# Kernel tuning notes

Measured on AMD Instinct MI355X. Metric: run time of the kernel, lower is better.

## Reference

```python
import jax, jax.numpy as jnp
import numpy as np

B = 8192
FL = 96      # feature_len
K = 3        # dynamic filter kernel size
NOUT = 2
EPS = 1e-5
P = (K - 1) // 2

def _lrelu(x):
    return jnp.where(x >= 0, x, 0.1 * x)

def _conv1d(x, w, b):
    # x: [b,1,L], w: [1,1,3], b: [1]; padding=1, stride=1
    y = jax.lax.conv_general_dilated(x, w, (1,), [(1, 1)], dimension_numbers=('NCH', 'OIH', 'NCH'))
    return y + b[None, :, None]

def _bn(y, g, be, m, v):
    # eval-mode BatchNorm1d with running stats
    return (y - m) / jnp.sqrt(v + EPS) * g + be


def setup_inputs() -> dict:
    key = jax.random.key(0)
    ks = jax.random.split(key, 40)
    d = {'x': jax.random.normal(ks[0], (B, 576), jnp.float32)}
    # trans_layer: 6 conv1d (1->1, k=3)
    for i in range(6):
        d[f'cw{i+1}'] = jax.random.normal(ks[1 + i], (1, 1, 3), jnp.float32) * 0.4
        d[f'cb{i+1}'] = jax.random.normal(ks[7 + i], (1,), jnp.float32) * 0.1
    # fusion_layer.de_dimen: Linear(FL -> K*K)
    d['de_W'] = jax.random.normal(ks[13], (K * K, FL), jnp.float32) * 0.1
    d['de_b'] = jnp.zeros((K * K,), jnp.float32)
    # reshape_layer: Linear(2*FL -> 3*FL) + BN
    d['rs_W'] = jax.random.normal(ks[14], (3 * FL, 2 * FL), jnp.float32) * 0.07
    d['rs_b'] = jnp.zeros((3 * FL,), jnp.float32)
    d['rs_g'] = 1.0 + 0.1 * jax.random.normal(ks[15], (3 * FL,), jnp.float32)
    d['rs_be'] = 0.1 * jax.random.normal(ks[16], (3 * FL,), jnp.float32)
    d['rs_m'] = 0.05 * jax.random.normal(ks[17], (3 * FL,), jnp.float32)
    d['rs_v'] = jax.random.uniform(ks[18], (3 * FL,), jnp.float32, 0.5, 1.5)
    # classifier_shallow: Linear(6*FL -> 3*FL) + BN + ReLU + Linear(3*FL -> NOUT)
    d['cl_W1'] = jax.random.normal(ks[19], (3 * FL, 6 * FL), jnp.float32) * 0.05
    d['cl_b1'] = jnp.zeros((3 * FL,), jnp.float32)
    d['cl_g'] = 1.0 + 0.1 * jax.random.normal(ks[20], (3 * FL,), jnp.float32)
    d['cl_be'] = 0.1 * jax.random.normal(ks[21], (3 * FL,), jnp.float32)
    d['cl_m'] = 0.05 * jax.random.normal(ks[22], (3 * FL,), jnp.float32)
    d['cl_v'] = jax.random.uniform(ks[23], (3 * FL,), jnp.float32, 0.5, 1.5)
    d['cl_W2'] = jax.random.normal(ks[24], (NOUT, 3 * FL), jnp.float32) * 0.05
    d['cl_b2'] = jnp.zeros((NOUT,), jnp.float32)
    return d


def reference(x, cw1, cb1, cw2, cb2, cw3, cb3, cw4, cb4, cw5, cb5, cw6, cb6,
              de_W, de_b, rs_W, rs_b, rs_g, rs_be, rs_m, rs_v,
              cl_W1, cl_b1, cl_g, cl_be, cl_m, cl_v, cl_W2, cl_b2):
    def trans(c):  # c: [b,1,3*FL] -> three [b,1,FL]
        s1, s2, s3 = c[..., :FL], c[..., FL:2 * FL], c[..., 2 * FL:]
        x1 = _lrelu(_conv1d(s1, cw1, cb1))
        x2 = _lrelu(_conv1d(s2, cw2, cb2))
        x3 = _lrelu(_conv1d(s3, cw3, cb3))
        return (_lrelu(_conv1d(x1, cw4, cb4)),
                _lrelu(_conv1d(x2, cw5, cb5)),
                _lrelu(_conv1d(x3, cw6, cb6)))

    def fusion(arm, x86, bert):  # each [b,1,FL]
        b = arm.shape[0]
        # c==1 so matmul(s_1^T, s_2) is a per-sample outer product: [b,FL,FL]
        m = _lrelu(jnp.einsum('bl,bm->blm', arm[:, 0], x86[:, 0]))
        # per-sample 3x3 dynamic filter from bert embedding
        s3 = _lrelu(bert[:, 0] @ de_W.T + de_b).reshape(b, 1, K, K)
        fe = jax.lax.conv_general_dilated(
            m.reshape(1, b, FL, FL), s3, (1, 1), [(P, P), (P, P)],
            feature_group_count=b, dimension_numbers=('NCHW', 'OIHW', 'NCHW'))
        fe = _lrelu(fe).reshape(b, FL, FL)
        # AvgPool1d(FL) == mean over last dim (and over rows for the permuted map)
        return jnp.concatenate([fe.mean(axis=2), fe.mean(axis=1)], axis=1)  # [b,2*FL]

    def resh(e):
        return _lrelu(_bn(e @ rs_W.T + rs_b, rs_g, rs_be, rs_m, rs_v))

    xu = x[:, None, :]  # unsqueeze(dim=1)
    c1, c2 = xu[..., :3 * FL], xu[..., 3 * FL:]
    e1 = resh(fusion(*trans(c1))) + c1[:, 0]
    e2 = resh(fusion(*trans(c2))) + c2[:, 0]
    ce = jnp.concatenate([e1, e2], axis=1)  # [b,6*FL]
    # Dropout is identity in eval mode
    h = jax.nn.relu(_bn(ce @ cl_W1.T + cl_b1, cl_g, cl_be, cl_m, cl_v))
    return h @ cl_W2.T + cl_b2  # [b,NOUT]
```

## Files before the change

kernel.cpp:

```cpp
#include <hip/hip_runtime.h>
#include <hip/hip_bf16.h>
#include <math.h>

#define FLn 96
#define SEG 288
#define EPRE_DIM 192
#define EPS_BN 1e-5f

typedef __attribute__((ext_vector_type(8))) short short8;
typedef __attribute__((ext_vector_type(4))) float floatx4;

__device__ __forceinline__ float lrelu(float v) { return fmaxf(v, 0.1f * v); }
__device__ __forceinline__ short f2bf(float f) {
  __hip_bfloat16 h = __float2bfloat16(f);
  return *reinterpret_cast<short*>(&h);
}

__global__ __launch_bounds__(256) void k0_swz(
    const float* __restrict__ rsW, const float* __restrict__ clW1,
    short* __restrict__ wB2s, short* __restrict__ wB3s) {
  int idx = blockIdx.x * 256 + threadIdx.x;
  int stride = gridDim.x * 256;
  for (int d = idx; d < 18 * 6 * 512; d += stride) {
    int j = d & 7, lane = (d >> 3) & 63, t = d >> 9;
    int kf = t % 6, nf = t / 6;
    int n = nf * 16 + (lane & 15);
    int k = kf * 32 + (lane >> 4) * 8 + j;
    wB2s[d] = f2bf(rsW[n * 192 + k]);
  }
  for (int d = idx; d < 18 * 18 * 512; d += stride) {
    int j = d & 7, lane = (d >> 3) & 63, t = d >> 9;
    int kf = t % 18, nt = t / 18;
    int n = nt * 16 + (lane & 15);
    int k = kf * 32 + (lane >> 4) * 8 + j;
    wB3s[d] = f2bf(clW1[n * 576 + k]);
  }
}

#define O_CIN 0
#define O_ST1 288
#define O_APP 576
#define O_ANP 674
#define O_XPP 772
#define O_XNP 870
#define O_BERT 968
#define O_WKER 1064
#define O_ABF 1088
#define O_BBF 1472
#define O_RP 0
#define SLICE 2048

__global__ __launch_bounds__(256) void k1_persample(
    const float* __restrict__ x,
    const float* __restrict__ cw1, const float* __restrict__ cb1,
    const float* __restrict__ cw2, const float* __restrict__ cb2,
    const float* __restrict__ cw3, const float* __restrict__ cb3,
    const float* __restrict__ cw4, const float* __restrict__ cb4,
    const float* __restrict__ cw5, const float* __restrict__ cb5,
    const float* __restrict__ cw6, const float* __restrict__ cb6,
    const float* __restrict__ deW, const float* __restrict__ deb,
    short* __restrict__ epre_s) {
  __shared__ float sl[4 * SLICE];
  const int tid = threadIdx.x;
  const int wave = tid >> 6;
  const int lane = tid & 63;
  const int quad = lane >> 4;
  const int l16 = lane & 15;
  const int unit = blockIdx.x * 4 + wave;
  float* S = sl + wave * SLICE;
  short* Ssh = (short*)S;
  const float* xrow = x + (size_t)(unit >> 1) * 576 + (unit & 1) * 288;

  const float a0w0 = cw1[0], a0w1 = cw1[1], a0w2 = cw1[2], a0b = cb1[0];
  const float a1w0 = cw2[0], a1w1 = cw2[1], a1w2 = cw2[2], a1b = cb2[0];
  const float a2w0 = cw3[0], a2w1 = cw3[1], a2w2 = cw3[2], a2b = cb3[0];
  const float b0w0 = cw4[0], b0w1 = cw4[1], b0w2 = cw4[2], b0b = cb4[0];
  const float b1w0 = cw5[0], b1w1 = cw5[1], b1w2 = cw5[2], b1b = cb5[0];
  const float b2w0 = cw6[0], b2w1 = cw6[1], b2w2 = cw6[2], b2b = cb6[0];

  for (int t4 = lane; t4 < 72; t4 += 64)
    *(float4*)&S[O_CIN + 4 * t4] = ((const float4*)xrow)[t4];
  if (lane < 8) S[576 + 98 * (lane >> 1) + (lane & 1) * 97] = 0.f;

  for (int t = lane; t < SEG; t += 64) {
    bool g1 = t >= 96, g2 = t >= 192;
    float wa = g2 ? a2w0 : (g1 ? a1w0 : a0w0);
    float wb = g2 ? a2w1 : (g1 ? a1w1 : a0w1);
    float wc = g2 ? a2w2 : (g1 ? a1w2 : a0w2);
    float bb = g2 ? a2b  : (g1 ? a1b  : a0b);
    int p = t - (g2 ? 192 : (g1 ? 96 : 0));
    float l = p > 0 ? S[O_CIN + t - 1] : 0.f;
    float m = S[O_CIN + t];
    float r = p < FLn - 1 ? S[O_CIN + t + 1] : 0.f;
    S[O_ST1 + t] = lrelu(fmaf(wa, l, fmaf(wb, m, fmaf(wc, r, bb))));
  }
  for (int t = lane; t < SEG; t += 64) {
    bool g1 = t >= 96, g2 = t >= 192;
    float wa = g2 ? b2w0 : (g1 ? b1w0 : b0w0);
    float wb = g2 ? b2w1 : (g1 ? b1w1 : b0w1);
    float wc = g2 ? b2w2 : (g1 ? b1w2 : b0w2);
    float bb = g2 ? b2b  : (g1 ? b1b  : b0b);
    int p = t - (g2 ? 192 : (g1 ? 96 : 0));
    float l = p > 0 ? S[O_ST1 + t - 1] : 0.f;
    float m = S[O_ST1 + t];
    float r = p < FLn - 1 ? S[O_ST1 + t + 1] : 0.f;
    float v = lrelu(fmaf(wa, l, fmaf(wb, m, fmaf(wc, r, bb))));
    if (!g1) {
      S[O_APP + 1 + p] = fmaxf(v, 0.1f * v);
      S[O_ANP + 1 + p] = fminf(v, 0.1f * v);
    } else if (!g2) {
      S[O_XPP + 1 + p] = fmaxf(v, 0.f);
      S[O_XNP + 1 + p] = fminf(v, 0.f);
    } else {
      S[O_BERT + p] = v;
    }
  }
  if (quad < 3) {
    float bv[6];
#pragma unroll
    for (int k = 0; k < 6; ++k) bv[k] = S[O_BERT + l16 + 16 * k];
#pragma unroll
    for (int oi = 0; oi < 3; ++oi) {
      int o = quad * 3 + oi;
      float p = 0.f;
#pragma unroll
      for (int k = 0; k < 6; ++k) p = fmaf(bv[k], deW[o * 96 + l16 + 16 * k], p);
      p += __shfl_xor(p, 1, 16);
      p += __shfl_xor(p, 2, 16);
      p += __shfl_xor(p, 4, 16);
      p += __shfl_xor(p, 8, 16);
      if (l16 == 0) S[O_WKER + o] = lrelu(p + deb[o]);
    }
  }
  float w9[9];
#pragma unroll
  for (int q = 0; q < 9; ++q) w9[q] = S[O_WKER + q];

  for (int t = lane; t < 96; t += 64) {
    float xp0 = S[O_XPP + t], xp1 = S[O_XPP + t + 1], xp2 = S[O_XPP + t + 2];
    float xn0 = S[O_XNP + t], xn1 = S[O_XNP + t + 1], xn2 = S[O_XNP + t + 2];
    short8 b;
#pragma unroll
    for (int d = 0; d < 3; ++d) {
      float cp = fmaf(w9[3 * d], xp0, fmaf(w9[3 * d + 1], xp1, w9[3 * d + 2] * xp2));
      float cn = fmaf(w9[3 * d], xn0, fmaf(w9[3 * d + 1], xn1, w9[3 * d + 2] * xn2));
      b[d] = f2bf(cp);
      b[3 + d] = f2bf(cn);
    }
    b[6] = 0; b[7] = 0;
    *(short8*)&Ssh[2 * O_BBF + t * 8] = b;
  }
  for (int m = lane; m < 96; m += 64) {
    short8 a;
    a[0] = f2bf(S[O_APP + m]);
    a[1] = f2bf(S[O_APP + m + 1]);
    a[2] = f2bf(S[O_APP + m + 2]);
    a[3] = f2bf(S[O_ANP + m]);
    a[4] = f2bf(S[O_ANP + m + 1]);
    a[5] = f2bf(S[O_ANP + m + 2]);
    a[6] = 0; a[7] = 0;
    *(short8*)&Ssh[2 * O_ABF + m * 8] = a;
  }

  short8 aF[6];
#pragma unroll
  for (int mt = 0; mt < 6; ++mt) {
    short8 t = *(const short8*)&Ssh[2 * O_ABF + (mt * 16 + l16) * 8];
#pragma unroll
    for (int j = 0; j < 8; ++j) aF[mt][j] = (quad == 0) ? t[j] : (short)0;
  }

  float rowpart[6][4];
#pragma unroll
  for (int mt = 0; mt < 6; ++mt)
#pragma unroll
    for (int r = 0; r < 4; ++r) rowpart[mt][r] = 0.f;
  float cs[6];
#pragma unroll
  for (int s = 0; s < 6; ++s) cs[s] = 0.f;

#pragma unroll
  for (int s = 0; s < 6; ++s) {
    short8 tb = *(const short8*)&Ssh[2 * O_BBF + (s * 16 + l16) * 8];
    short8 bF;
#pragma unroll
    for (int j = 0; j < 8; ++j) bF[j] = (quad == 0) ? tb[j] : (short)0;
    floatx4 accv[6];
#pragma unroll
    for (int mt = 0; mt < 6; ++mt)
      accv[mt] = __builtin_amdgcn_mfma_f32_16x16x32_bf16(
          aF[mt], bF, (floatx4){0.f, 0.f, 0.f, 0.f}, 0, 0, 0);
#pragma unroll
    for (int mt = 0; mt < 6; ++mt) {
#pragma unroll
      for (int r = 0; r < 4; ++r) {
        float sv = accv[mt][r];
        float f = fmaxf(sv, 0.1f * sv);
        rowpart[mt][r] += f;
        cs[s] += f;
      }
    }
  }

#pragma unroll
  for (int mt = 0; mt < 6; ++mt)
    *(float4*)&S[O_RP + (quad * 6 + mt) * 68 + l16 * 4] =
        make_float4(rowpart[mt][0], rowpart[mt][1], rowpart[mt][2], rowpart[mt][3]);

  const int g = unit >> 4;
  const int u15 = unit & 15;
  short* eb = epre_s + (size_t)g * 6 * 512;
  for (int i = lane; i < 96; i += 64) {
    int gg = ((i >> 2) & 3) * 6 + (i >> 4);
    int r = i & 3;
    float s = 0.f;
#pragma unroll
    for (int l = 0; l < 16; ++l) s += S[O_RP + gg * 68 + l * 4 + r];
    int kf = i >> 5, rem = i & 31, q = rem >> 3, j = rem & 7;
    eb[kf * 512 + (q * 16 + u15) * 8 + j] = f2bf(s * (1.f / FLn));
  }
#pragma unroll
  for (int s = 0; s < 6; ++s) {
    float v = cs[s];
    v += __shfl_xor(v, 16, 64);
    v += __shfl_xor(v, 32, 64);
    if (quad == 0) {
      int kidx = 96 + s * 16 + l16;
      int kf = kidx >> 5, rem = kidx & 31, q = rem >> 3, j = rem & 7;
      eb[kf * 512 + (q * 16 + u15) * 8 + j] = f2bf(v * (1.f / FLn));
    }
  }
}

__global__ __launch_bounds__(512) void k6_fused_tail(
    const short* __restrict__ epre_s, const short* __restrict__ wB2s,
    const short* __restrict__ wB3s, const float* __restrict__ x,
    const float* __restrict__ rsb, const float* __restrict__ rsg,
    const float* __restrict__ rsbe, const float* __restrict__ rsm,
    const float* __restrict__ rsv,
    const float* __restrict__ clb1, const float* __restrict__ clg,
    const float* __restrict__ clbe, const float* __restrict__ clm,
    const float* __restrict__ clv,
    const float* __restrict__ clW2, const float* __restrict__ clb2,
    float* __restrict__ out) {
  __shared__ short ceT[16 * 584];
  __shared__ float scr[8 * 32];
  const int tid = threadIdx.x;
  const int w = tid >> 6;
  const int lane = tid & 63;
  const int quad = lane >> 4;
  const int l16 = lane & 15;
  const int s0 = blockIdx.x * 16;

  const int mt = w & 1;
  const int ng = w >> 1;
  short8 aF[6];
  {
    const short* arow = epre_s + (size_t)(blockIdx.x * 2 + mt) * 6 * 512 + lane * 8;
#pragma unroll
    for (int kf = 0; kf < 6; ++kf) aF[kf] = *(const short8*)(arow + kf * 512);
  }

  for (int nf = ng; nf < 18; nf += 4) {
    const short* brow = wB2s + (size_t)nf * 6 * 512 + lane * 8;
    floatx4 acc = (floatx4){0.f, 0.f, 0.f, 0.f};
#pragma unroll
    for (int kf = 0; kf < 6; ++kf) {
      short8 bF = *(const short8*)(brow + kf * 512);
      acc = __builtin_amdgcn_mfma_f32_16x16x32_bf16(aF[kf], bF, acc, 0, 0, 0);
    }
    const int n = nf * 16 + l16;
    const float sc = rsg[n] * rsqrtf(rsv[n] + EPS_BN);
    const float vb = rsb[n], mu = rsm[n], vbe = rsbe[n];
#pragma unroll
    for (int r = 0; r < 4; ++r) {
      int um = mt * 16 + quad * 4 + r;
      int trow = um >> 1;
      int cc = (um & 1) * 288 + n;
      float y = acc[r] + vb;
      float o = (y - mu) * sc + vbe;
      float e = lrelu(o) + x[(size_t)(s0 + trow) * 576 + cc];
      ceT[trow * 584 + cc] = f2bf(e);
    }
  }
  __syncthreads();

  float p0[4], p1[4];
#pragma unroll
  for (int r = 0; r < 4; ++r) { p0[r] = 0.f; p1[r] = 0.f; }

  for (int nt = w; nt < 18; nt += 8) {
    const short* brow = wB3s + (size_t)nt * 18 * 512 + lane * 8;
    floatx4 acc = (floatx4){0.f, 0.f, 0.f, 0.f};
#pragma unroll
    for (int kf = 0; kf < 18; ++kf) {
      short8 cF = *(const short8*)&ceT[l16 * 584 + kf * 32 + quad * 8];
      short8 bF = *(const short8*)(brow + kf * 512);
      acc = __builtin_amdgcn_mfma_f32_16x16x32_bf16(cF, bF, acc, 0, 0, 0);
    }
    const int n = nt * 16 + l16;
    const float sc = clg[n] * rsqrtf(clv[n] + EPS_BN);
    const float vb = clb1[n], mu = clm[n], vbe = clbe[n];
    const float w2a = clW2[n], w2b = clW2[288 + n];
#pragma unroll
    for (int r = 0; r < 4; ++r) {
      float y = acc[r] + vb;
      float hh = fmaxf((y - mu) * sc + vbe, 0.f);
      p0[r] = fmaf(hh, w2a, p0[r]);
      p1[r] = fmaf(hh, w2b, p1[r]);
    }
  }
#pragma unroll
  for (int r = 0; r < 4; ++r) {
#pragma unroll
    for (int off = 1; off < 16; off <<= 1) {
      p0[r] += __shfl_xor(p0[r], off, 64);
      p1[r] += __shfl_xor(p1[r], off, 64);
    }
  }
  if (l16 == 0) {
#pragma unroll
    for (int r = 0; r < 4; ++r) {
      scr[w * 32 + (quad * 4 + r) * 2 + 0] = p0[r];
      scr[w * 32 + (quad * 4 + r) * 2 + 1] = p1[r];
    }
  }
  __syncthreads();
  if (tid < 32) {
    int row = tid >> 1, o = tid & 1;
    float s = 0.f;
#pragma unroll
    for (int g = 0; g < 8; ++g) s += scr[g * 32 + row * 2 + o];
    out[(size_t)(s0 + row) * 2 + o] = s + clb2[o];
  }
}

extern "C" void kernel_launch(void* const* d_in, const int* in_sizes, int n_in,
                              void* d_out, int out_size, void* d_ws, size_t ws_size,
                              hipStream_t stream) {
  const float* x   = (const float*)d_in[0];
  const float* cw1 = (const float*)d_in[1];  const float* cb1 = (const float*)d_in[2];
  const float* cw2 = (const float*)d_in[3];  const float* cb2 = (const float*)d_in[4];
  const float* cw3 = (const float*)d_in[5];  const float* cb3 = (const float*)d_in[6];
  const float* cw4 = (const float*)d_in[7];  const float* cb4 = (const float*)d_in[8];
  const float* cw5 = (const float*)d_in[9];  const float* cb5 = (const float*)d_in[10];
  const float* cw6 = (const float*)d_in[11]; const float* cb6 = (const float*)d_in[12];
  const float* deW = (const float*)d_in[13]; const float* deb = (const float*)d_in[14];
  const float* rsW = (const float*)d_in[15]; const float* rsb = (const float*)d_in[16];
  const float* rsg = (const float*)d_in[17]; const float* rsbe = (const float*)d_in[18];
  const float* rsm = (const float*)d_in[19]; const float* rsv = (const float*)d_in[20];
  const float* clW1 = (const float*)d_in[21]; const float* clb1 = (const float*)d_in[22];
  const float* clg = (const float*)d_in[23]; const float* clbe = (const float*)d_in[24];
  const float* clm = (const float*)d_in[25]; const float* clv = (const float*)d_in[26];
  const float* clW2 = (const float*)d_in[27]; const float* clb2 = (const float*)d_in[28];

  short* ws    = (short*)d_ws;
  short* epre_s = ws;
  short* wB2s  = ws + 16384 * 192;
  short* wB3s  = wB2s + 18 * 6 * 512;

  hipLaunchKernelGGL(k0_swz, dim3(128), dim3(256), 0, stream,
                     rsW, clW1, wB2s, wB3s);
  hipLaunchKernelGGL(k1_persample, dim3(4096), dim3(256), 0, stream, x,
                     cw1, cb1, cw2, cb2, cw3, cb3, cw4, cb4, cw5, cb5, cw6, cb6,
                     deW, deb, epre_s);
  hipLaunchKernelGGL(k6_fused_tail, dim3(512), dim3(512), 0, stream,
                     epre_s, wB2s, wB3s, x,
                     rsb, rsg, rsbe, rsm, rsv,
                     clb1, clg, clbe, clm, clv,
                     clW2, clb2, (float*)d_out);
}
```

Baseline: 201.5 us.

## Fuse weight swizzle into per-sample kernel, shrink LDS slice, drop quad masking

Removes the separate weight-swizzle launch by having each k1 thread convert one element of the rsW/clW1 bf16 fragments, which drops one kernel launch. The LDS slice is shrunk by overlaying the bf16 fragment buffers on the input area, and launch bounds now request higher occupancy. Quad masking of MFMA operands is removed; instead the dynamic kernel is scaled by 0.25, presumably because the nonzero fragment data is now replicated across all four quads and the MFMA sum counts it four times. The leaky-relu accumulation is rewritten with two-wide float vectors. The overlaid LDS regions and the bf16 scaling assumptions bring correctness risk.

```diff
diff --git a/kernel.cpp b/kernel.cpp
--- a/kernel.cpp
+++ b/kernel.cpp
@@ -9,32 +9,12 @@
 
 typedef __attribute__((ext_vector_type(8))) short short8;
 typedef __attribute__((ext_vector_type(4))) float floatx4;
+typedef float v2f __attribute__((ext_vector_type(2)));
 
 __device__ __forceinline__ float lrelu(float v) { return fmaxf(v, 0.1f * v); }
 __device__ __forceinline__ short f2bf(float f) {
   __hip_bfloat16 h = __float2bfloat16(f);
   return *reinterpret_cast<short*>(&h);
-}
-
-__global__ __launch_bounds__(256) void k0_swz(
-    const float* __restrict__ rsW, const float* __restrict__ clW1,
-    short* __restrict__ wB2s, short* __restrict__ wB3s) {
-  int idx = blockIdx.x * 256 + threadIdx.x;
-  int stride = gridDim.x * 256;
-  for (int d = idx; d < 18 * 6 * 512; d += stride) {
-    int j = d & 7, lane = (d >> 3) & 63, t = d >> 9;
-    int kf = t % 6, nf = t / 6;
-    int n = nf * 16 + (lane & 15);
-    int k = kf * 32 + (lane >> 4) * 8 + j;
-    wB2s[d] = f2bf(rsW[n * 192 + k]);
-  }
-  for (int d = idx; d < 18 * 18 * 512; d += stride) {
-    int j = d & 7, lane = (d >> 3) & 63, t = d >> 9;
-    int kf = t % 18, nt = t / 18;
-    int n = nt * 16 + (lane & 15);
-    int k = kf * 32 + (lane >> 4) * 8 + j;
-    wB3s[d] = f2bf(clW1[n * 576 + k]);
-  }
 }
 
 #define O_CIN 0
@@ -45,12 +25,12 @@
 #define O_XNP 870
 #define O_BERT 968
 #define O_WKER 1064
-#define O_ABF 1088
-#define O_BBF 1472
+#define O_ABF 0
+#define O_BBF 384
 #define O_RP 0
-#define SLICE 2048
-
-__global__ __launch_bounds__(256) void k1_persample(
+#define SLICE 1664
+
+__global__ __launch_bounds__(256, 6) void k1_persample(
     const float* __restrict__ x,
     const float* __restrict__ cw1, const float* __restrict__ cb1,
     const float* __restrict__ cw2, const float* __restrict__ cb2,
@@ -59,6 +39,8 @@
     const float* __restrict__ cw5, const float* __restrict__ cb5,
     const float* __restrict__ cw6, const float* __restrict__ cb6,
     const float* __restrict__ deW, const float* __restrict__ deb,
+    const float* __restrict__ rsW, const float* __restrict__ clW1,
+    short* __restrict__ wB2s, short* __restrict__ wB3s,
     short* __restrict__ epre_s) {
   __shared__ float sl[4 * SLICE];
   const int tid = threadIdx.x;
@@ -70,6 +52,24 @@
   float* S = sl + wave * SLICE;
   short* Ssh = (short*)S;
   const float* xrow = x + (size_t)(unit >> 1) * 576 + (unit & 1) * 288;
+
+  {
+    int d = blockIdx.x * 256 + tid;
+    if (d < 18 * 6 * 512) {
+      int j = d & 7, ln = (d >> 3) & 63, t = d >> 9;
+      int kf = t % 6, nf = t / 6;
+      int n = nf * 16 + (ln & 15);
+      int k = kf * 32 + (ln >> 4) * 8 + j;
+      wB2s[d] = f2bf(rsW[n * 192 + k]);
+    }
+    if (d < 18 * 18 * 512) {
+      int j = d & 7, ln = (d >> 3) & 63, t = d >> 9;
+      int kf = t % 18, nt = t / 18;
+      int n = nt * 16 + (ln & 15);
+      int k = kf * 32 + (ln >> 4) * 8 + j;
+      wB3s[d] = f2bf(clW1[n * 576 + k]);
+    }
+  }
 
   const float a0w0 = cw1[0], a0w1 = cw1[1], a0w2 = cw1[2], a0b = cb1[0];
   const float a1w0 = cw2[0], a1w1 = cw2[1], a1w2 = cw2[2], a1b = cb2[0];
@@ -132,24 +132,7 @@
       if (l16 == 0) S[O_WKER + o] = lrelu(p + deb[o]);
     }
   }
-  float w9[9];
-#pragma unroll
-  for (int q = 0; q < 9; ++q) w9[q] = S[O_WKER + q];
-
-  for (int t = lane; t < 96; t += 64) {
-    float xp0 = S[O_XPP + t], xp1 = S[O_XPP + t + 1], xp2 = S[O_XPP + t + 2];
-    float xn0 = S[O_XNP + t], xn1 = S[O_XNP + t + 1], xn2 = S[O_XNP + t + 2];
-    short8 b;
-#pragma unroll
-    for (int d = 0; d < 3; ++d) {
-      float cp = fmaf(w9[3 * d], xp0, fmaf(w9[3 * d + 1], xp1, w9[3 * d + 2] * xp2));
-      float cn = fmaf(w9[3 * d], xn0, fmaf(w9[3 * d + 1], xn1, w9[3 * d + 2] * xn2));
-      b[d] = f2bf(cp);
-      b[3 + d] = f2bf(cn);
-    }
-    b[6] = 0; b[7] = 0;
-    *(short8*)&Ssh[2 * O_BBF + t * 8] = b;
-  }
+
   for (int m = lane; m < 96; m += 64) {
     short8 a;
     a[0] = f2bf(S[O_APP + m]);
@@ -161,51 +144,66 @@
     a[6] = 0; a[7] = 0;
     *(short8*)&Ssh[2 * O_ABF + m * 8] = a;
   }
+  float w9[9];
+#pragma unroll
+  for (int q = 0; q < 9; ++q) w9[q] = 0.25f * S[O_WKER + q];
+  for (int t = lane; t < 96; t += 64) {
+    float xp0 = S[O_XPP + t], xp1 = S[O_XPP + t + 1], xp2 = S[O_XPP + t + 2];
+    float xn0 = S[O_XNP + t], xn1 = S[O_XNP + t + 1], xn2 = S[O_XNP + t + 2];
+    short8 b;
+#pragma unroll
+    for (int d = 0; d < 3; ++d) {
+      float cp = fmaf(w9[3 * d], xp0, fmaf(w9[3 * d + 1], xp1, w9[3 * d + 2] * xp2));
+      float cn = fmaf(w9[3 * d], xn0, fmaf(w9[3 * d + 1], xn1, w9[3 * d + 2] * xn2));
+      b[d] = f2bf(cp);
+      b[3 + d] = f2bf(cn);
+    }
+    b[6] = 0; b[7] = 0;
+    *(short8*)&Ssh[2 * O_BBF + t * 8] = b;
+  }
 
   short8 aF[6];
 #pragma unroll
+  for (int mt = 0; mt < 6; ++mt)
+    aF[mt] = *(const short8*)&Ssh[2 * O_ABF + (mt * 16 + l16) * 8];
+
+  v2f rp2[6][2];
+#pragma unroll
   for (int mt = 0; mt < 6; ++mt) {
-    short8 t = *(const short8*)&Ssh[2 * O_ABF + (mt * 16 + l16) * 8];
-#pragma unroll
-    for (int j = 0; j < 8; ++j) aF[mt][j] = (quad == 0) ? t[j] : (short)0;
-  }
-
-  float rowpart[6][4];
-#pragma unroll
-  for (int mt = 0; mt < 6; ++mt)
-#pragma unroll
-    for (int r = 0; r < 4; ++r) rowpart[mt][r] = 0.f;
+    rp2[mt][0] = (v2f){0.f, 0.f};
+    rp2[mt][1] = (v2f){0.f, 0.f};
+  }
   float cs[6];
-#pragma unroll
-  for (int s = 0; s < 6; ++s) cs[s] = 0.f;
 
 #pragma unroll
   for (int s = 0; s < 6; ++s) {
-    short8 tb = *(const short8*)&Ssh[2 * O_BBF + (s * 16 + l16) * 8];
-    short8 bF;
-#pragma unroll
-    for (int j = 0; j < 8; ++j) bF[j] = (quad == 0) ? tb[j] : (short)0;
+    short8 bF = *(const short8*)&Ssh[2 * O_BBF + (s * 16 + l16) * 8];
     floatx4 accv[6];
 #pragma unroll
     for (int mt = 0; mt < 6; ++mt)
       accv[mt] = __builtin_amdgcn_mfma_f32_16x16x32_bf16(
           aF[mt], bF, (floatx4){0.f, 0.f, 0.f, 0.f}, 0, 0, 0);
+    v2f csl = (v2f){0.f, 0.f};
 #pragma unroll
     for (int mt = 0; mt < 6; ++mt) {
-#pragma unroll
-      for (int r = 0; r < 4; ++r) {
-        float sv = accv[mt][r];
-        float f = fmaxf(sv, 0.1f * sv);
-        rowpart[mt][r] += f;
-        cs[s] += f;
-      }
-    }
+      v2f lo = (v2f){accv[mt][0], accv[mt][1]};
+      v2f hi = (v2f){accv[mt][2], accv[mt][3]};
+      v2f tl = 0.1f * lo;
+      v2f th = 0.1f * hi;
+      v2f fl, fh;
+      fl.x = fmaxf(lo.x, tl.x); fl.y = fmaxf(lo.y, tl.y);
+      fh.x = fmaxf(hi.x, th.x); fh.y = fmaxf(hi.y, th.y);
+      rp2[mt][0] += fl;
+      rp2[mt][1] += fh;
+      csl += fl + fh;
+    }
+    cs[s] = csl.x + csl.y;
   }
 
 #pragma unroll
   for (int mt = 0; mt < 6; ++mt)
     *(float4*)&S[O_RP + (quad * 6 + mt) * 68 + l16 * 4] =
-        make_float4(rowpart[mt][0], rowpart[mt][1], rowpart[mt][2], rowpart[mt][3]);
+        make_float4(rp2[mt][0].x, rp2[mt][0].y, rp2[mt][1].x, rp2[mt][1].y);
 
   const int g = unit >> 4;
   const int u15 = unit & 15;
@@ -354,16 +352,14 @@
   const float* clm = (const float*)d_in[25]; const float* clv = (const float*)d_in[26];
   const float* clW2 = (const float*)d_in[27]; const float* clb2 = (const float*)d_in[28];
 
-  short* ws    = (short*)d_ws;
+  short* ws     = (short*)d_ws;
   short* epre_s = ws;
-  short* wB2s  = ws + 16384 * 192;
-  short* wB3s  = wB2s + 18 * 6 * 512;
-
-  hipLaunchKernelGGL(k0_swz, dim3(128), dim3(256), 0, stream,
-                     rsW, clW1, wB2s, wB3s);
+  short* wB2s   = ws + 16384 * 192;
+  short* wB3s   = wB2s + 18 * 6 * 512;
+
   hipLaunchKernelGGL(k1_persample, dim3(4096), dim3(256), 0, stream, x,
                      cw1, cb1, cw2, cb2, cw3, cb3, cw4, cb4, cw5, cb5, cw6, cb6,
-                     deW, deb, epre_s);
+                     deW, deb, rsW, clW1, wB2s, wB3s, epre_s);
   hipLaunchKernelGGL(k6_fused_tail, dim3(512), dim3(512), 0, stream,
                      epre_s, wB2s, wB3s, x,
                      rsb, rsg, rsbe, rsm, rsv,
```

Result: slower. 422.1 us (+109.5%).
